# Optimization experiments

Hardware: AMD Instinct MI355X
Metric: run time of the kernel (lower is better)

The kernel has to match this reference:

```python
import jax, jax.numpy as jnp
import numpy as np

H = 16
D_MODEL = 1024
D_K = D_MODEL // H
NEG_INF = -1e9


def setup_inputs() -> dict:
    key = jax.random.key(0)
    ks = jax.random.split(key, 11)
    B, S = 4, 2048
    scale = 1.0 / np.sqrt(D_MODEL)
    inp = {
        "query": jax.random.normal(ks[0], (B, S, D_MODEL), jnp.float32),
        "key": jax.random.normal(ks[1], (B, S, D_MODEL), jnp.float32),
        "value": jax.random.normal(ks[2], (B, S, D_MODEL), jnp.float32),
        "Wq": jax.random.normal(ks[3], (D_MODEL, D_MODEL), jnp.float32) * scale,
        "bq": jnp.zeros((D_MODEL,), jnp.float32),
        "Wk": jax.random.normal(ks[4], (D_MODEL, D_MODEL), jnp.float32) * scale,
        "bk": jnp.zeros((D_MODEL,), jnp.float32),
        "Wv": jax.random.normal(ks[5], (D_MODEL, D_MODEL), jnp.float32) * scale,
        "bv": jnp.zeros((D_MODEL,), jnp.float32),
        "Wo": jax.random.normal(ks[6], (D_MODEL, D_MODEL), jnp.float32) * scale,
        "bo": jnp.zeros((D_MODEL,), jnp.float32),
    }
    return inp


def _split_heads(x):
    # [B, S, D] -> [B, H, S, D_K]
    B, S, _ = x.shape
    return x.reshape(B, S, H, D_K).transpose(0, 2, 1, 3)


def reference(query, key, value, Wq, bq, Wk, bk, Wv, bv, Wo, bo):
    # Linear projections (torch Linear: y = x @ W.T + b)
    q = _split_heads(query @ Wq.T + bq)   # [B,H,S,Dk]
    k = _split_heads(key @ Wk.T + bk)
    v = _split_heads(value @ Wv.T + bv)

    S = q.shape[2]
    scores = jnp.einsum("bhqd,bhkd->bhqk", q, k) / jnp.sqrt(jnp.float32(D_K))
    causal = jnp.tril(jnp.ones((S, S), jnp.bool_))  # [S,S]
    scores = jnp.where(causal[None, None], scores, NEG_INF)
    p_attn = jax.nn.softmax(scores, axis=-1)  # dropout p=0.0 (eval)
    x = jnp.einsum("bhqk,bhkd->bhqd", p_attn, v)  # [B,H,S,Dk]
    B = x.shape[0]
    x = x.transpose(0, 2, 1, 3).reshape(B, S, H * D_K)
    return x @ Wo.T + bo
```

## Files before the change

### kernel.cpp

```cpp
#include <hip/hip_runtime.h>
#include <hip/hip_bf16.h>
#include <stdint.h>

#define NH 16
#define SEQ 2048
#define DMODEL 1024
#define DK 64
#define BATCH 4
#define M_TOT 8192

#define LOG2E 1.44269504088896f
#define QSCALE (0.125f * LOG2E)

typedef short v8bf __attribute__((ext_vector_type(8)));
typedef float f32x4 __attribute__((ext_vector_type(4)));

__device__ __forceinline__ unsigned pack_bf2(float a, float b) {
  union { __hip_bfloat162 h; unsigned u; } v;
  v.h = __float22bfloat162_rn(make_float2(a, b));
  return v.u;
}

__device__ __forceinline__ unsigned short f2bf(float f) {
  union { __hip_bfloat16 h; unsigned short u; } v;
  v.h = __float2bfloat16(f);
  return v.u;
}

__device__ __forceinline__ void async_load16(const void* g, void* l) {
  __builtin_amdgcn_global_load_lds(
      (const __attribute__((address_space(1))) unsigned int*)(uintptr_t)g,
      (__attribute__((address_space(3))) unsigned int*)(unsigned)(uintptr_t)l,
      16, 0, 0);
}

__global__ __launch_bounds__(256)
void cvt_kernel(const float* __restrict__ q, const float* __restrict__ k,
                const float* __restrict__ v,
                const float* __restrict__ wq, const float* __restrict__ wk,
                const float* __restrict__ wv, const float* __restrict__ wo,
                unsigned short* __restrict__ oq, unsigned short* __restrict__ ok,
                unsigned short* __restrict__ ov,
                unsigned short* __restrict__ owq, unsigned short* __restrict__ owk,
                unsigned short* __restrict__ owv, unsigned short* __restrict__ owo)
{
  const size_t XN = (size_t)M_TOT * DMODEL;
  const size_t WN = (size_t)DMODEL * DMODEL;
  const float* s; unsigned short* d; size_t n;
  switch (blockIdx.y) {
    case 0: s = q;  d = oq;  n = XN; break;
    case 1: s = k;  d = ok;  n = XN; break;
    case 2: s = v;  d = ov;  n = XN; break;
    case 3: s = wq; d = owq; n = WN; break;
    case 4: s = wk; d = owk; n = WN; break;
    case 5: s = wv; d = owv; n = WN; break;
    default: s = wo; d = owo; n = WN; break;
  }
  for (size_t i = ((size_t)blockIdx.x * 256 + threadIdx.x) * 8; i < n;
       i += (size_t)gridDim.x * 256 * 8) {
    float4 a = *(const float4*)(s + i);
    float4 b = *(const float4*)(s + i + 4);
    uint4 p = { pack_bf2(a.x, a.y), pack_bf2(a.z, a.w),
                pack_bf2(b.x, b.y), pack_bf2(b.z, b.w) };
    *(uint4*)(d + i) = p;
  }
}

__global__ __launch_bounds__(256, 2)
void proj_bf16_kernel(const unsigned short* __restrict__ Xq,
                      const unsigned short* __restrict__ Xk,
                      const unsigned short* __restrict__ Xv,
                      const unsigned short* __restrict__ Wqc,
                      const unsigned short* __restrict__ Wkc,
                      const unsigned short* __restrict__ Wvc,
                      const float* __restrict__ bq, const float* __restrict__ bk,
                      const float* __restrict__ bv,
                      unsigned short* __restrict__ Qp, unsigned short* __restrict__ Kp,
                      unsigned short* __restrict__ Vp)
{
  const int z = blockIdx.z;
  const unsigned short* A = (z == 0) ? Xq : (z == 1) ? Xk : Xv;
  const unsigned short* W = (z == 0) ? Wqc : (z == 1) ? Wkc : Wvc;
  const float* bias = (z == 0) ? bq : (z == 1) ? bk : bv;
  unsigned short* Out = (z == 0) ? Qp : (z == 1) ? Kp : Vp;
  const float scale = (z == 0) ? QSCALE : 1.0f;

  __shared__ unsigned short As[128 * 64];
  __shared__ unsigned short Bs[128 * 64];

  const int tid  = threadIdx.x;
  const int m0   = blockIdx.x * 128;
  const int n0   = blockIdx.y * 128;
  const int lane = tid & 63;
  const int wave = tid >> 6;
  const int quad = lane >> 4;
  const int l16  = lane & 15;
  const int wm   = (wave >> 1) * 64;
  const int wn   = (wave & 1) * 64;
  const int lrow = lane >> 3;
  const int lcol = lane & 7;

  f32x4 acc[4][4];
#pragma unroll
  for (int i = 0; i < 4; ++i)
#pragma unroll
    for (int j = 0; j < 4; ++j) acc[i][j] = (f32x4){0.f, 0.f, 0.f, 0.f};

  for (int k0 = 0; k0 < DMODEL; k0 += 64) {
#pragma unroll
    for (int i = 0; i < 4; ++i) {
      int row = wave * 32 + i * 8 + lrow;
      int gc = (lcol ^ (row & 7)) * 8;
      async_load16(A + (size_t)(m0 + row) * DMODEL + k0 + gc, &As[(wave * 32 + i * 8) * 64]);
      async_load16(W + (size_t)(n0 + row) * DMODEL + k0 + gc, &Bs[(wave * 32 + i * 8) * 64]);
    }
    __syncthreads();

#pragma unroll
    for (int ks = 0; ks < 2; ++ks) {
      v8bf af[4], bf[4];
#pragma unroll
      for (int i = 0; i < 4; ++i)
        af[i] = *(const v8bf*)&As[(wm + i * 16 + l16) * 64 + ((ks * 4 + quad) ^ (l16 & 7)) * 8];
#pragma unroll
      for (int j = 0; j < 4; ++j)
        bf[j] = *(const v8bf*)&Bs[(wn + j * 16 + l16) * 64 + ((ks * 4 + quad) ^ (l16 & 7)) * 8];
#pragma unroll
      for (int i = 0; i < 4; ++i)
#pragma unroll
        for (int j = 0; j < 4; ++j)
          acc[i][j] = __builtin_amdgcn_mfma_f32_16x16x32_bf16(af[i], bf[j], acc[i][j], 0, 0, 0);
    }
    __syncthreads();
  }

  if (z < 2) {
#pragma unroll
    for (int j = 0; j < 4; ++j) {
      int colg = n0 + wn + j * 16 + l16;
      float bj = bias[colg];
      int h = colg >> 6, d = colg & 63;
#pragma unroll
      for (int i = 0; i < 4; ++i) {
#pragma unroll
        for (int reg = 0; reg < 4; ++reg) {
          int mrow = m0 + wm + i * 16 + quad * 4 + reg;
          int bb = mrow >> 11, ss = mrow & 2047;
          float val = (acc[i][j][reg] + bj) * scale;
          Out[(((size_t)bb * NH + h) * SEQ + ss) * DK + d] = f2bf(val);
        }
      }
    }
  } else {
#pragma unroll
    for (int j = 0; j < 4; ++j) {
      int colg = n0 + wn + j * 16 + l16;
      float bj = bias[colg];
      int h = colg >> 6, d = colg & 63;
#pragma unroll
      for (int i = 0; i < 4; ++i) {
        int mrow = m0 + wm + i * 16 + quad * 4;
        int bb = mrow >> 11, ss = mrow & 2047;
        uint2 pk = { pack_bf2(acc[i][j][0] + bj, acc[i][j][1] + bj),
                     pack_bf2(acc[i][j][2] + bj, acc[i][j][3] + bj) };
        *(uint2*)(Out + (((size_t)bb * NH + h) * DK + d) * SEQ + ss) = pk;
      }
    }
  }
}

__global__ __launch_bounds__(256, 2)
void attn_kernel(const unsigned short* __restrict__ Qp,
                 const unsigned short* __restrict__ Kp,
                 const unsigned short* __restrict__ VTp,
                 unsigned short* __restrict__ Xout)
{
  const int y  = blockIdx.y;
  const int r  = y & 3, jj = y >> 2;
  const int qt = (jj == 0) ? (15 - r) : (jj == 1) ? (8 + r) : (jj == 2) ? (7 - r) : r;
  const int bh = blockIdx.x;
  const int b  = bh >> 4, h = bh & 15;

  const unsigned short* Qb = Qp  + ((size_t)bh * SEQ + qt * 128) * DK;
  const unsigned short* Kb = Kp  + (size_t)bh * SEQ * DK;
  const unsigned short* Vb = VTp + (size_t)bh * DK * SEQ;

  __shared__ unsigned short Ks[2][64 * 64];
  __shared__ unsigned short VTs[2][64 * 64];

  const int tid  = threadIdx.x;
  const int lane = tid & 63, wave = tid >> 6;
  const int quad = lane >> 4, l16 = lane & 15;
  const int row_lo = qt * 128 + wave * 32;

  const int laneA = l16 + 16 * ((2 * quad) & 3);
  const int laneB = l16 + 16 * ((2 * quad + 1) & 3);
  const bool loq = (quad < 2);

  v8bf qf[2][2];
#pragma unroll
  for (int rf = 0; rf < 2; ++rf)
#pragma unroll
    for (int ks = 0; ks < 2; ++ks)
      qf[rf][ks] = *(const v8bf*)(Qb + (size_t)(wave * 32 + rf * 16 + l16) * DK + ks * 32 + quad * 8);

  float lp2[2];
  f32x4 o[2][4];
  lp2[0] = lp2[1] = 0.f;
#pragma unroll
  for (int rf = 0; rf < 2; ++rf)
#pragma unroll
    for (int df = 0; df < 4; ++df) o[rf][df] = (f32x4){0.f, 0.f, 0.f, 0.f};

  const int nchunk = 2 * (qt + 1);
  const int lrow = lane >> 3;
  const int lcol = lane & 7;

#pragma unroll
  for (int is = 0; is < 2; ++is) {
    int row = wave * 16 + is * 8 + lrow;
    int cK = ((lcol ^ (row & 7)) * 8);
    async_load16(Kb + (size_t)row * DK + cK, &Ks[0][(wave * 16 + is * 8) * 64]);
    async_load16(Vb + (size_t)row * SEQ + cK, &VTs[0][(wave * 16 + is * 8) * 64]);
  }
  __syncthreads();

  for (int c = 0; c < nchunk; ++c) {
    const int buf = c & 1;
    const int kb  = c * 64;

    if (c + 1 < nchunk) {
      const int kb2 = kb + 64;
#pragma unroll
      for (int is = 0; is < 2; ++is) {
        int row = wave * 16 + is * 8 + lrow;
        int cc = ((lcol ^ (row & 7)) * 8);
        async_load16(Kb + (size_t)(kb2 + row) * DK + cc, &Ks[buf ^ 1][(wave * 16 + is * 8) * 64]);
        async_load16(Vb + (size_t)row * SEQ + kb2 + cc, &VTs[buf ^ 1][(wave * 16 + is * 8) * 64]);
      }
    }

    if (kb <= row_lo + 31) {
      f32x4 s2[2][4];
#pragma unroll
      for (int rf = 0; rf < 2; ++rf)
#pragma unroll
        for (int nf = 0; nf < 4; ++nf) s2[rf][nf] = (f32x4){0.f, 0.f, 0.f, 0.f};
      __builtin_amdgcn_s_setprio(1);
#pragma unroll
      for (int ks = 0; ks < 2; ++ks)
#pragma unroll
        for (int nf = 0; nf < 4; ++nf) {
          v8bf kf = *(const v8bf*)&Ks[buf][(nf * 16 + l16) * 64 + ((ks * 4 + quad) ^ (l16 & 7)) * 8];
          s2[0][nf] = __builtin_amdgcn_mfma_f32_16x16x32_bf16(kf, qf[0][ks], s2[0][nf], 0, 0, 0);
          s2[1][nf] = __builtin_amdgcn_mfma_f32_16x16x32_bf16(kf, qf[1][ks], s2[1][nf], 0, 0, 0);
        }
      __builtin_amdgcn_s_setprio(0);

      if (kb + 63 > row_lo) {
#pragma unroll
        for (int rf = 0; rf < 2; ++rf) {
          int qrow = row_lo + rf * 16 + l16;
#pragma unroll
          for (int nf = 0; nf < 4; ++nf) {
            int kcol = kb + nf * 16 + quad * 4;
#pragma unroll
            for (int reg = 0; reg < 4; ++reg)
              if (kcol + reg > qrow) s2[rf][nf][reg] = -1e30f;
          }
        }
      }

#pragma unroll
      for (int rf = 0; rf < 2; ++rf) {
#pragma unroll
        for (int nf = 0; nf < 4; ++nf)
#pragma unroll
          for (int reg = 0; reg < 4; ++reg)
            s2[rf][nf][reg] = __builtin_amdgcn_exp2f(s2[rf][nf][reg]);
#pragma unroll
        for (int nf = 0; nf < 4; ++nf)
          lp2[rf] += (s2[rf][nf][0] + s2[rf][nf][1]) + (s2[rf][nf][2] + s2[rf][nf][3]);

        int w[4][2];
#pragma unroll
        for (int nf = 0; nf < 4; ++nf) {
          w[nf][0] = (int)pack_bf2(s2[rf][nf][0], s2[rf][nf][1]);
          w[nf][1] = (int)pack_bf2(s2[rf][nf][2], s2[rf][nf][3]);
        }

#pragma unroll
        for (int ks = 0; ks < 2; ++ks) {
          union { int wi[4]; v8bf v; } pf;
#pragma unroll
          for (int t = 0; t < 4; ++t) {
            int srcl = (t < 2) ? laneA : laneB;
            int r1 = __shfl(w[2 * ks][t & 1], srcl);
            int r2 = __shfl(w[2 * ks + 1][t & 1], srcl);
            pf.wi[t] = loq ? r1 : r2;
          }
          __builtin_amdgcn_s_setprio(1);
#pragma unroll
          for (int df = 0; df < 4; ++df) {
            v8bf vf = *(const v8bf*)&VTs[buf][(df * 16 + l16) * 64 + ((ks * 4 + quad) ^ (l16 & 7)) * 8];
            o[rf][df] = __builtin_amdgcn_mfma_f32_16x16x32_bf16(pf.v, vf, o[rf][df], 0, 0, 0);
          }
          __builtin_amdgcn_s_setprio(0);
        }
      }
    }
    __syncthreads();
  }

#pragma unroll
  for (int rf = 0; rf < 2; ++rf) {
    lp2[rf] += __shfl_xor(lp2[rf], 16);
    lp2[rf] += __shfl_xor(lp2[rf], 32);
    float inv = 1.0f / lp2[rf];
    float invd[4];
#pragma unroll
    for (int reg = 0; reg < 4; ++reg) invd[reg] = __shfl(inv, quad * 4 + reg);
#pragma unroll
    for (int df = 0; df < 4; ++df)
#pragma unroll
      for (int reg = 0; reg < 4; ++reg) {
        int qrow = row_lo + rf * 16 + quad * 4 + reg;
        Xout[(size_t)(b * SEQ + qrow) * DMODEL + h * DK + df * 16 + l16] =
            f2bf(o[rf][df][reg] * invd[reg]);
      }
  }
}

__global__ __launch_bounds__(256, 2)
void oproj_kernel(const unsigned short* __restrict__ Xa,
                  const unsigned short* __restrict__ Woc,
                  const float* __restrict__ bo,
                  float* __restrict__ Out)
{
  __shared__ unsigned short As[128 * 64];
  __shared__ unsigned short Bs[128 * 64];

  const int tid  = threadIdx.x;
  const int m0   = blockIdx.x * 128;
  const int n0   = blockIdx.y * 128;
  const int lane = tid & 63;
  const int wave = tid >> 6;
  const int quad = lane >> 4;
  const int l16  = lane & 15;
  const int wm   = (wave >> 1) * 64;
  const int wn   = (wave & 1) * 64;
  const int lrow = lane >> 3;
  const int lcol = lane & 7;

  f32x4 acc[4][4];
#pragma unroll
  for (int i = 0; i < 4; ++i)
#pragma unroll
    for (int j = 0; j < 4; ++j) acc[i][j] = (f32x4){0.f, 0.f, 0.f, 0.f};

  for (int k0 = 0; k0 < DMODEL; k0 += 64) {
#pragma unroll
    for (int i = 0; i < 4; ++i) {
      int row = wave * 32 + i * 8 + lrow;
      int gc = (lcol ^ (row & 7)) * 8;
      async_load16(Xa  + (size_t)(m0 + row) * DMODEL + k0 + gc, &As[(wave * 32 + i * 8) * 64]);
      async_load16(Woc + (size_t)(n0 + row) * DMODEL + k0 + gc, &Bs[(wave * 32 + i * 8) * 64]);
    }
    __syncthreads();

#pragma unroll
    for (int ks = 0; ks < 2; ++ks) {
      v8bf af[4], bf[4];
#pragma unroll
      for (int i = 0; i < 4; ++i)
        af[i] = *(const v8bf*)&As[(wm + i * 16 + l16) * 64 + ((ks * 4 + quad) ^ (l16 & 7)) * 8];
#pragma unroll
      for (int j = 0; j < 4; ++j)
        bf[j] = *(const v8bf*)&Bs[(wn + j * 16 + l16) * 64 + ((ks * 4 + quad) ^ (l16 & 7)) * 8];
#pragma unroll
      for (int i = 0; i < 4; ++i)
#pragma unroll
        for (int j = 0; j < 4; ++j)
          acc[i][j] = __builtin_amdgcn_mfma_f32_16x16x32_bf16(af[i], bf[j], acc[i][j], 0, 0, 0);
    }
    __syncthreads();
  }

#pragma unroll
  for (int j = 0; j < 4; ++j) {
    int colg = n0 + wn + j * 16 + l16;
    float bj = bo[colg];
#pragma unroll
    for (int i = 0; i < 4; ++i) {
#pragma unroll
      for (int reg = 0; reg < 4; ++reg) {
        int mrow = m0 + wm + i * 16 + quad * 4 + reg;
        Out[(size_t)mrow * DMODEL + colg] = acc[i][j][reg] + bj;
      }
    }
  }
}

extern "C" void kernel_launch(void* const* d_in, const int* in_sizes, int n_in,
                              void* d_out, int out_size, void* d_ws, size_t ws_size,
                              hipStream_t stream)
{
  const float* query = (const float*)d_in[0];
  const float* key   = (const float*)d_in[1];
  const float* value = (const float*)d_in[2];
  const float* Wq = (const float*)d_in[3];
  const float* bq = (const float*)d_in[4];
  const float* Wk = (const float*)d_in[5];
  const float* bk = (const float*)d_in[6];
  const float* Wv = (const float*)d_in[7];
  const float* bv = (const float*)d_in[8];
  const float* Wo = (const float*)d_in[9];
  const float* bo = (const float*)d_in[10];

  const size_t tsz = (size_t)M_TOT * DMODEL;
  const size_t wsz = (size_t)DMODEL * DMODEL;
  unsigned short* Qp  = (unsigned short*)d_ws;
  unsigned short* Kp  = Qp + tsz;
  unsigned short* Vp  = Kp + tsz;
  unsigned short* Xa  = Vp + tsz;
  unsigned short* Xqc = Xa + tsz;
  unsigned short* Xkc = Xqc + tsz;
  unsigned short* Xvc = Xkc + tsz;
  unsigned short* Wqc = Xvc + tsz;
  unsigned short* Wkc = Wqc + wsz;
  unsigned short* Wvc = Wkc + wsz;
  unsigned short* Woc = Wvc + wsz;

  cvt_kernel<<<dim3(1024, 7), 256, 0, stream>>>(query, key, value, Wq, Wk, Wv, Wo,
                                                Xqc, Xkc, Xvc, Wqc, Wkc, Wvc, Woc);
  proj_bf16_kernel<<<dim3(64, 8, 3), 256, 0, stream>>>(Xqc, Xkc, Xvc, Wqc, Wkc, Wvc,
                                                       bq, bk, bv, Qp, Kp, Vp);
  attn_kernel<<<dim3(64, 16), 256, 0, stream>>>(Qp, Kp, Vp, Xa);
  oproj_kernel<<<dim3(64, 8), 256, 0, stream>>>(Xa, Woc, bo, (float*)d_out);
}
```

Before: 307.1 us.

## Load K and V fragments directly from global memory, dropping LDS staging

The attention kernel stops staging K and V tiles through double-buffered shared memory with async loads and block-wide barriers. Each wave now reads its MFMA K and V^T fragments straight from global memory, relying on L2/cache reuse, and iterates only over the key chunks its own rows need. This removes the LDS traffic and __syncthreads stalls and lets waves proceed independently, but each of the four waves now fetches the same K/V data separately, and global load latency is no longer hidden by explicit prefetch.

Measured after the change: 375.1 us. 22.1% more time.

```diff
diff --git a/kernel.cpp b/kernel.cpp
--- a/kernel.cpp
+++ b/kernel.cpp
@@ -185,9 +185,6 @@
   const unsigned short* Kb = Kp  + (size_t)bh * SEQ * DK;
   const unsigned short* Vb = VTp + (size_t)bh * DK * SEQ;
 
-  __shared__ unsigned short Ks[2][64 * 64];
-  __shared__ unsigned short VTs[2][64 * 64];
-
   const int tid  = threadIdx.x;
   const int lane = tid & 63, wave = tid >> 6;
   const int quad = lane >> 4, l16 = lane & 15;
@@ -212,104 +209,89 @@
 #pragma unroll
     for (int df = 0; df < 4; ++df) o[rf][df] = (f32x4){0.f, 0.f, 0.f, 0.f};
 
-  const int nchunk = 2 * (qt + 1);
-  const int lrow = lane >> 3;
-  const int lcol = lane & 7;
-
-#pragma unroll
-  for (int is = 0; is < 2; ++is) {
-    int row = wave * 16 + is * 8 + lrow;
-    int cK = ((lcol ^ (row & 7)) * 8);
-    async_load16(Kb + (size_t)row * DK + cK, &Ks[0][(wave * 16 + is * 8) * 64]);
-    async_load16(Vb + (size_t)row * SEQ + cK, &VTs[0][(wave * 16 + is * 8) * 64]);
-  }
-  __syncthreads();
-
-  for (int c = 0; c < nchunk; ++c) {
-    const int buf = c & 1;
-    const int kb  = c * 64;
-
-    if (c + 1 < nchunk) {
-      const int kb2 = kb + 64;
-#pragma unroll
-      for (int is = 0; is < 2; ++is) {
-        int row = wave * 16 + is * 8 + lrow;
-        int cc = ((lcol ^ (row & 7)) * 8);
-        async_load16(Kb + (size_t)(kb2 + row) * DK + cc, &Ks[buf ^ 1][(wave * 16 + is * 8) * 64]);
-        async_load16(Vb + (size_t)row * SEQ + kb2 + cc, &VTs[buf ^ 1][(wave * 16 + is * 8) * 64]);
-      }
-    }
-
-    if (kb <= row_lo + 31) {
-      f32x4 s2[2][4];
-#pragma unroll
-      for (int rf = 0; rf < 2; ++rf)
-#pragma unroll
-        for (int nf = 0; nf < 4; ++nf) s2[rf][nf] = (f32x4){0.f, 0.f, 0.f, 0.f};
-      __builtin_amdgcn_s_setprio(1);
-#pragma unroll
-      for (int ks = 0; ks < 2; ++ks)
+  const int cmax = (row_lo + 31) >> 6;
+
+  for (int c = 0; c <= cmax; ++c) {
+    const int kb = c * 64;
+
+    v8bf kf[2][4];
+#pragma unroll
+    for (int ks = 0; ks < 2; ++ks)
+#pragma unroll
+      for (int nf = 0; nf < 4; ++nf)
+        kf[ks][nf] = *(const v8bf*)(Kb + (size_t)(kb + nf * 16 + l16) * DK + ks * 32 + quad * 8);
+
+    f32x4 s2[2][4];
+#pragma unroll
+    for (int rf = 0; rf < 2; ++rf)
+#pragma unroll
+      for (int nf = 0; nf < 4; ++nf) s2[rf][nf] = (f32x4){0.f, 0.f, 0.f, 0.f};
+    __builtin_amdgcn_s_setprio(1);
+#pragma unroll
+    for (int ks = 0; ks < 2; ++ks)
+#pragma unroll
+      for (int nf = 0; nf < 4; ++nf) {
+        s2[0][nf] = __builtin_amdgcn_mfma_f32_16x16x32_bf16(kf[ks][nf], qf[0][ks], s2[0][nf], 0, 0, 0);
+        s2[1][nf] = __builtin_amdgcn_mfma_f32_16x16x32_bf16(kf[ks][nf], qf[1][ks], s2[1][nf], 0, 0, 0);
+      }
+    __builtin_amdgcn_s_setprio(0);
+
+    v8bf vf[2][4];
+#pragma unroll
+    for (int ks = 0; ks < 2; ++ks)
+#pragma unroll
+      for (int df = 0; df < 4; ++df)
+        vf[ks][df] = *(const v8bf*)(Vb + (size_t)(df * 16 + l16) * SEQ + kb + ks * 32 + quad * 8);
+
+    if (kb + 63 > row_lo) {
+#pragma unroll
+      for (int rf = 0; rf < 2; ++rf) {
+        int qrow = row_lo + rf * 16 + l16;
 #pragma unroll
         for (int nf = 0; nf < 4; ++nf) {
-          v8bf kf = *(const v8bf*)&Ks[buf][(nf * 16 + l16) * 64 + ((ks * 4 + quad) ^ (l16 & 7)) * 8];
-          s2[0][nf] = __builtin_amdgcn_mfma_f32_16x16x32_bf16(kf, qf[0][ks], s2[0][nf], 0, 0, 0);
-          s2[1][nf] = __builtin_amdgcn_mfma_f32_16x16x32_bf16(kf, qf[1][ks], s2[1][nf], 0, 0, 0);
+          int kcol = kb + nf * 16 + quad * 4;
+#pragma unroll
+          for (int reg = 0; reg < 4; ++reg)
+            if (kcol + reg > qrow) s2[rf][nf][reg] = -1e30f;
         }
-      __builtin_amdgcn_s_setprio(0);
-
-      if (kb + 63 > row_lo) {
-#pragma unroll
-        for (int rf = 0; rf < 2; ++rf) {
-          int qrow = row_lo + rf * 16 + l16;
-#pragma unroll
-          for (int nf = 0; nf < 4; ++nf) {
-            int kcol = kb + nf * 16 + quad * 4;
-#pragma unroll
-            for (int reg = 0; reg < 4; ++reg)
-              if (kcol + reg > qrow) s2[rf][nf][reg] = -1e30f;
-          }
+      }
+    }
+
+#pragma unroll
+    for (int rf = 0; rf < 2; ++rf) {
+#pragma unroll
+      for (int nf = 0; nf < 4; ++nf)
+#pragma unroll
+        for (int reg = 0; reg < 4; ++reg)
+          s2[rf][nf][reg] = __builtin_amdgcn_exp2f(s2[rf][nf][reg]);
+#pragma unroll
+      for (int nf = 0; nf < 4; ++nf)
+        lp2[rf] += (s2[rf][nf][0] + s2[rf][nf][1]) + (s2[rf][nf][2] + s2[rf][nf][3]);
+
+      int w[4][2];
+#pragma unroll
+      for (int nf = 0; nf < 4; ++nf) {
+        w[nf][0] = (int)pack_bf2(s2[rf][nf][0], s2[rf][nf][1]);
+        w[nf][1] = (int)pack_bf2(s2[rf][nf][2], s2[rf][nf][3]);
+      }
+
+#pragma unroll
+      for (int ks = 0; ks < 2; ++ks) {
+        union { int wi[4]; v8bf v; } pf;
+#pragma unroll
+        for (int t = 0; t < 4; ++t) {
+          int srcl = (t < 2) ? laneA : laneB;
+          int r1 = __shfl(w[2 * ks][t & 1], srcl);
+          int r2 = __shfl(w[2 * ks + 1][t & 1], srcl);
+          pf.wi[t] = loq ? r1 : r2;
         }
-      }
-
-#pragma unroll
-      for (int rf = 0; rf < 2; ++rf) {
-#pragma unroll
-        for (int nf = 0; nf < 4; ++nf)
-#pragma unroll
-          for (int reg = 0; reg < 4; ++reg)
-            s2[rf][nf][reg] = __builtin_amdgcn_exp2f(s2[rf][nf][reg]);
-#pragma unroll
-        for (int nf = 0; nf < 4; ++nf)
-          lp2[rf] += (s2[rf][nf][0] + s2[rf][nf][1]) + (s2[rf][nf][2] + s2[rf][nf][3]);
-
-        int w[4][2];
-#pragma unroll
-        for (int nf = 0; nf < 4; ++nf) {
-          w[nf][0] = (int)pack_bf2(s2[rf][nf][0], s2[rf][nf][1]);
-          w[nf][1] = (int)pack_bf2(s2[rf][nf][2], s2[rf][nf][3]);
-        }
-
-#pragma unroll
-        for (int ks = 0; ks < 2; ++ks) {
-          union { int wi[4]; v8bf v; } pf;
-#pragma unroll
-          for (int t = 0; t < 4; ++t) {
-            int srcl = (t < 2) ? laneA : laneB;
-            int r1 = __shfl(w[2 * ks][t & 1], srcl);
-            int r2 = __shfl(w[2 * ks + 1][t & 1], srcl);
-            pf.wi[t] = loq ? r1 : r2;
-          }
-          __builtin_amdgcn_s_setprio(1);
-#pragma unroll
-          for (int df = 0; df < 4; ++df) {
-            v8bf vf = *(const v8bf*)&VTs[buf][(df * 16 + l16) * 64 + ((ks * 4 + quad) ^ (l16 & 7)) * 8];
-            o[rf][df] = __builtin_amdgcn_mfma_f32_16x16x32_bf16(pf.v, vf, o[rf][df], 0, 0, 0);
-          }
-          __builtin_amdgcn_s_setprio(0);
-        }
-      }
-    }
-    __syncthreads();
+        __builtin_amdgcn_s_setprio(1);
+#pragma unroll
+        for (int df = 0; df < 4; ++df)
+          o[rf][df] = __builtin_amdgcn_mfma_f32_16x16x32_bf16(pf.v, vf[ks][df], o[rf][df], 0, 0, 0);
+        __builtin_amdgcn_s_setprio(0);
+      }
+    }
   }
 
 #pragma unroll
```
